# Kernel optimization log

Measured on AMD Instinct MI355X. Metric: run time of the kernel, lower is better.

The kernel has to match this reference:

```python
import jax, jax.numpy as jnp
import numpy as np

PLANES = ((0, 1), (0, 2), (0, 3), (1, 2), (1, 3), (2, 3))
LOOKBACK = 8
EPS = 1e-6


def phi(x):
    # LeakyReLU(negative_slope=0.01) + 1.0
    return jnp.where(x >= 0, x, 0.01 * x) + 1.0


def ga_embed(x, scalar_bias, vector_scale, vector_bias, bivector_weight):
    # x: [B, L, 4] -> M: [B, L, 11] = [scalar(1), vectors(4), bivectors(6)]
    scalar = jnp.broadcast_to(1.0 + scalar_bias, x.shape[:2] + (1,)).astype(x.dtype)
    vec = x * vector_scale + vector_bias
    biv = jnp.stack(
        [bivector_weight[k] * (x[..., i] - x[..., j]) for k, (i, j) in enumerate(PLANES)],
        axis=-1,
    )
    return jnp.concatenate([scalar, vec, biv], axis=-1)


def linear_attention(M, WQ, WK, WV):
    # Vectorized form of the per-timestep loop: for output t (t in [LOOKBACK, L)),
    # window is K/V[t-LOOKBACK : t]. q_t . S = sum_l (q_t . k_l) v_l, so we contract
    # scores first and never materialize the [B,T,H,H] S tensor.
    L = M.shape[1]
    T = L - LOOKBACK
    Q = phi(M @ WQ.T)   # [B, L, H]
    K = phi(M @ WK.T)
    V = M @ WV.T
    q = Q[:, LOOKBACK:]                                             # [B, T, H]
    K_win = jnp.stack([K[:, l:l + T] for l in range(LOOKBACK)], axis=2)  # [B, T, Lb, H]
    V_win = jnp.stack([V[:, l:l + T] for l in range(LOOKBACK)], axis=2)  # [B, T, Lb, H]
    scores = jnp.einsum('bth,btlh->btl', q, K_win)                  # [B, T, Lb]
    Z = K_win.sum(axis=2)                                           # [B, T, H]
    num = jnp.einsum('btl,btlg->btg', scores, V_win)                # [B, T, H]
    den = jnp.sum(q * Z, axis=-1, keepdims=True) + EPS
    contexts = num / den
    weights = scores / (jnp.sum(scores, axis=-1, keepdims=True) + EPS)
    return contexts, weights


def head_apply(ctx, head_W, head_b):
    # LinearHead: proj(H -> 1) then squeeze(-1)
    return (ctx @ head_W.T + head_b)[..., 0]


def qonly_delta(M, s0, s1, WQ, WK, WV, head_W, head_b):
    # _delta_y_query_only_fixed: last query t = L-1, window [t-Lb, t)
    Dm = M.shape[-1]
    q = phi(M[:, -1] @ WQ.T)                 # [B, H]
    win = M[:, -1 - LOOKBACK:-1]             # [B, Lb, Dm]
    k_win = phi(win @ WK.T)
    v_win = win @ WV.T
    S = jnp.einsum('blh,blg->bhg', k_win, v_win)   # [B, H, H] (small)
    Z = k_win.sum(axis=1)                           # [B, H]
    mask = jnp.zeros((Dm,), M.dtype).at[s0:s1].set(1.0)
    h_imp = (jnp.abs(WQ) * mask[None, :]).sum(axis=1)
    h_mask = h_imp / (h_imp.max() + 1e-12)
    q_masked = q * (1.0 - h_mask)

    def out(qv):
        num = jnp.einsum('bh,bhg->bg', qv, S)
        den = jnp.sum(qv * Z, axis=-1, keepdims=True) + EPS
        return head_apply(num / den, head_W, head_b)

    return jnp.abs(out(q) - out(q_masked)).mean()


def setup_inputs() -> dict:
    key = jax.random.key(0)
    ks = jax.random.split(key, 10)
    B, L, H, Dm = 16, 4096, 128, 11
    x = jax.random.normal(ks[0], (B, L, 4), dtype=jnp.float32)
    scalar_bias = 0.1 * jax.random.normal(ks[1], (1,), dtype=jnp.float32)
    vector_scale = 1.0 + 0.1 * jax.random.normal(ks[2], (4,), dtype=jnp.float32)
    vector_bias = 0.1 * jax.random.normal(ks[3], (4,), dtype=jnp.float32)
    bivector_weight = 1.0 + 0.1 * jax.random.normal(ks[4], (6,), dtype=jnp.float32)
    s = 1.0 / np.sqrt(Dm)
    WQ = s * jax.random.normal(ks[5], (H, Dm), dtype=jnp.float32)
    WK = s * jax.random.normal(ks[6], (H, Dm), dtype=jnp.float32)
    WV = s * jax.random.normal(ks[7], (H, Dm), dtype=jnp.float32)
    head_W = (1.0 / np.sqrt(H)) * jax.random.normal(ks[8], (1, H), dtype=jnp.float32)
    head_b = 0.1 * jax.random.normal(ks[9], (1,), dtype=jnp.float32)
    return {"x": x, "scalar_bias": scalar_bias, "vector_scale": vector_scale,
            "vector_bias": vector_bias, "bivector_weight": bivector_weight,
            "WQ": WQ, "WK": WK, "WV": WV, "head_W": head_W, "head_b": head_b}


def reference(x, scalar_bias, vector_scale, vector_bias, bivector_weight, WQ, WK, WV, head_W, head_b):
    M = ga_embed(x, scalar_bias, vector_scale, vector_bias, bivector_weight)
    contexts, attention_weights = linear_attention(M, WQ, WK, WV)
    predictions = head_apply(contexts, head_W, head_b)

    # interpretability (no_grad in the original)
    Ms = jax.lax.stop_gradient(M)
    scalar_mag = jnp.abs(Ms[..., 0]).mean()
    vector_mag = jnp.abs(Ms[..., 1:5]).mean()
    biv_mag = jnp.abs(Ms[..., 5:]).mean()

    def ablate_delta(Mz):
        ctx, _ = linear_attention(Mz, WQ, WK, WV)
        return jnp.abs(predictions - head_apply(ctx, head_W, head_b)).mean()

    delta_scalar = ablate_delta(Ms.at[..., 0].set(0.0))
    delta_vectors = ablate_delta(Ms.at[..., 1:5].set(0.0))
    delta_biv = ablate_delta(Ms.at[..., 5:].set(0.0))

    Dm = M.shape[-1]
    q_scalar = qonly_delta(Ms, 0, 1, WQ, WK, WV, head_W, head_b)
    q_vector = qonly_delta(Ms, 1, 5, WQ, WK, WV, head_W, head_b)
    q_biv = qonly_delta(Ms, 5, Dm, WQ, WK, WV, head_W, head_b)

    interpretability = jnp.stack([scalar_mag, vector_mag, biv_mag,
                                  delta_scalar, delta_vectors, delta_biv,
                                  q_scalar, q_vector, q_biv])
    return predictions, attention_weights, interpretability
```

## Files before the change

### kernel.cpp

```cpp
#include <hip/hip_runtime.h>

#define B_ 16
#define L_ 4096
#define H_ 128
#define DM 11
#define LB 8
#define T_ (L_-LB)
#define TT 64
#define NTB (L_/TT)
#define NBLK (NTB*B_)
#define EPSC 1e-6f
#define MAGS_BASE 4096
#define QONLY_BASE 8192


__device__ __forceinline__ float phi_f(float a) { return fmaxf(a, 0.01f * a) + 1.f; }

__device__ __forceinline__ float4 phi4(float a, float b, float c, float d) {
  return make_float4(phi_f(a), phi_f(b), phi_f(c), phi_f(d));
}

__device__ __forceinline__ void ga_parts(const float4 xv, const float* __restrict__ vs4,
                                         const float* __restrict__ vb4,
                                         const float* __restrict__ bw6, float* __restrict__ r) {
  r[0] = xv.x * vs4[0] + vb4[0];
  r[1] = xv.y * vs4[1] + vb4[1];
  r[2] = xv.z * vs4[2] + vb4[2];
  r[3] = xv.w * vs4[3] + vb4[3];
  r[4] = bw6[0] * (xv.x - xv.y);
  r[5] = bw6[1] * (xv.x - xv.z);
  r[6] = bw6[2] * (xv.x - xv.w);
  r[7] = bw6[3] * (xv.y - xv.z);
  r[8] = bw6[4] * (xv.y - xv.w);
  r[9] = bw6[5] * (xv.z - xv.w);
}

__device__ __forceinline__ void dot2(const float* __restrict__ r, const float* __restrict__ w,
                                     float& dv, float& db) {
  dv = r[0] * w[1] + r[1] * w[2] + r[2] * w[3] + r[3] * w[4];
  db = r[4] * w[5] + r[5] * w[6] + r[6] * w[7] + r[7] * w[8] + r[8] * w[9] + r[9] * w[10];
}

__global__ __launch_bounds__(256) void attn_kernel(
    const float* __restrict__ x, const float* __restrict__ sbp,
    const float* __restrict__ vs, const float* __restrict__ vb,
    const float* __restrict__ bw, const float* __restrict__ WQ,
    const float* __restrict__ WK, const float* __restrict__ WV,
    const float* __restrict__ hW, const float* __restrict__ hb,
    float* __restrict__ out, float* __restrict__ ws)
{
  __shared__ float4 sK4[4][8][72];
  __shared__ float4 sU4[72];
  __shared__ float  sWVe[16];

  const int tid  = threadIdx.x;
  const int lane = tid & 63;
  const int hq   = __builtin_amdgcn_readfirstlane(tid >> 6);
  const int tile = blockIdx.x;
  const int b    = blockIdx.y;
  const int base = tile * TT;

  const float sb0 = sbp[0];
  const float m0c = 1.f + sb0;
  float vs4[4] = {vs[0], vs[1], vs[2], vs[3]};
  float vb4[4] = {vb[0], vb[1], vb[2], vb[3]};
  float bw6[6] = {bw[0], bw[1], bw[2], bw[3], bw[4], bw[5]};
  const float hb0 = hb[0];

  const float4* xb = (const float4*)x + (size_t)b * L_;

  float ms[10], mq[10], m2[10];
  ga_parts(xb[base + lane], vs4, vb4, bw6, ms);
  {
    int qp = base + lane + LB;
    if (qp < L_) ga_parts(xb[qp], vs4, vb4, bw6, mq);
    else { for (int i = 0; i < 10; ++i) mq[i] = 0.f; }
  }
  const bool has2 = (lane < LB);
  if (has2) {
    int p2 = base + 64 + lane;
    if (p2 < L_) ga_parts(xb[p2], vs4, vb4, bw6, m2);
    else { for (int i = 0; i < 10; ++i) m2[i] = 0.f; }
  }
  float magv = fabsf(ms[0]) + fabsf(ms[1]) + fabsf(ms[2]) + fabsf(ms[3]);
  float magb = fabsf(ms[4]) + fabsf(ms[5]) + fabsf(ms[6]) + fabsf(ms[7]) + fabsf(ms[8]) + fabsf(ms[9]);

  if (hq == 1 && lane < DM) {
    float a = 0.f;
    for (int g = 0; g < H_; ++g) a += WV[g * DM + lane] * hW[g];
    sWVe[lane] = a;
  }
  __syncthreads();

  if (hq == 0) {
    float wv[11];
#pragma unroll
    for (int d = 0; d < DM; ++d) wv[d] = sWVe[d];
    float dv, db;
    dot2(ms, wv, dv, db);
    float c0 = m0c * wv[0];
    sU4[lane] = make_float4(c0 + dv + db, dv + db, c0 + db, c0 + dv);
    if (has2) {
      dot2(m2, wv, dv, db);
      sU4[64 + lane] = make_float4(c0 + dv + db, dv + db, c0 + db, c0 + dv);
    }
  }

  float4 s4[8];
#pragma unroll
  for (int l = 0; l < 8; ++l) s4[l] = make_float4(0.f, 0.f, 0.f, 0.f);

  const float* __restrict__ WKq = WK + (hq * 32) * DM;
  const float* __restrict__ WQq = WQ + (hq * 32) * DM;

#pragma unroll 1
  for (int c = 0; c < 4; ++c) {
#pragma unroll
    for (int hl = 0; hl < 8; ++hl) {
      const float* wk = WKq + (c * 8 + hl) * DM;
      float dv, db;
      dot2(ms, wk, dv, db);
      float c0 = m0c * wk[0];
      float t1 = dv + db;
      sK4[hq][hl][lane] = phi4(c0 + t1, t1, c0 + db, c0 + dv);
    }
    if (has2) {
#pragma unroll
      for (int hl = 0; hl < 8; ++hl) {
        const float* wk = WKq + (c * 8 + hl) * DM;
        float dv, db;
        dot2(m2, wk, dv, db);
        float c0 = m0c * wk[0];
        float t1 = dv + db;
        sK4[hq][hl][64 + lane] = phi4(c0 + t1, t1, c0 + db, c0 + dv);
      }
    }
    __syncthreads();
#pragma unroll
    for (int hl = 0; hl < 8; ++hl) {
      const float* wq = WQq + (c * 8 + hl) * DM;
      float dv, db;
      dot2(mq, wq, dv, db);
      float c0 = m0c * wq[0];
      float t1 = dv + db;
      float4 q4 = phi4(c0 + t1, t1, c0 + db, c0 + dv);
#pragma unroll
      for (int l = 0; l < 8; ++l) {
        float4 k4 = sK4[hq][hl][lane + l];
        s4[l].x += q4.x * k4.x;
        s4[l].y += q4.y * k4.y;
        s4[l].z += q4.z * k4.z;
        s4[l].w += q4.w * k4.w;
      }
    }
    __syncthreads();
  }

  float4* scr = &sK4[0][0][0];
  if (hq != 0) {
    int off = (hq - 1) * 512 + lane * 8;
#pragma unroll
    for (int l = 0; l < 8; ++l) scr[off + (l ^ (lane & 7))] = s4[l];
  }
  __syncthreads();

  if (hq == 0) {
#pragma unroll
    for (int j = 0; j < 3; ++j) {
      int off = j * 512 + lane * 8;
#pragma unroll
      for (int l = 0; l < 8; ++l) {
        float4 v = scr[off + (l ^ (lane & 7))];
        s4[l].x += v.x; s4[l].y += v.y; s4[l].z += v.z; s4[l].w += v.w;
      }
    }
    float den0 = EPSC, den1 = EPSC, den2 = EPSC, den3 = EPSC;
    float num0 = 0.f, num1 = 0.f, num2 = 0.f, num3 = 0.f;
#pragma unroll
    for (int l = 0; l < 8; ++l) {
      float4 u4 = sU4[lane + l];
      den0 += s4[l].x; num0 += s4[l].x * u4.x;
      den1 += s4[l].y; num1 += s4[l].y * u4.y;
      den2 += s4[l].z; num2 += s4[l].z * u4.z;
      den3 += s4[l].w; num3 += s4[l].w * u4.w;
    }
    float p0 = hb0 + num0 / den0;
    float p1 = hb0 + num1 / den1;
    float p2 = hb0 + num2 / den2;
    float p3 = hb0 + num3 / den3;

    const int t = base + lane;
    const bool tvalid = (t < T_);
    if (tvalid) {
      out[(size_t)b * T_ + t] = p0;
      float inv = 1.f / den0;
      float4* wp = (float4*)(out + (size_t)B_ * T_ + ((size_t)b * T_ + t) * 8);
      wp[0] = make_float4(s4[0].x * inv, s4[1].x * inv, s4[2].x * inv, s4[3].x * inv);
      wp[1] = make_float4(s4[4].x * inv, s4[5].x * inv, s4[6].x * inv, s4[7].x * inv);
    }
    float d1 = tvalid ? fabsf(p0 - p1) : 0.f;
    float d2 = tvalid ? fabsf(p0 - p2) : 0.f;
    float d3 = tvalid ? fabsf(p0 - p3) : 0.f;
#pragma unroll
    for (int off = 32; off >= 1; off >>= 1) {
      d1 += __shfl_xor(d1, off);
      d2 += __shfl_xor(d2, off);
      d3 += __shfl_xor(d3, off);
      magv += __shfl_xor(magv, off);
      magb += __shfl_xor(magb, off);
    }
    if (lane == 0) {
      int bid = b * NTB + tile;
      ws[bid]             = d1;
      ws[1024 + bid]      = d2;
      ws[2048 + bid]      = d3;
      ws[MAGS_BASE + 2 * bid]     = magv;
      ws[MAGS_BASE + 2 * bid + 1] = magb;
    }
  }

  if (hq == 1 && tile == NTB - 1) {
    const int h0 = lane, h1 = lane + 64;
    float wq0[11], wq1[11], wk0[11], wk1[11], wv[11];
#pragma unroll
    for (int d = 0; d < DM; ++d) {
      wq0[d] = WQ[h0 * DM + d]; wq1[d] = WQ[h1 * DM + d];
      wk0[d] = WK[h0 * DM + d]; wk1[d] = WK[h1 * DM + d];
      wv[d]  = sWVe[d];
    }
    float A0 = 0.f, Z0 = 0.f, A1 = 0.f, Z1 = 0.f;
#pragma unroll
    for (int l = 0; l < LB; ++l) {
      float4 xv = xb[L_ - 1 - LB + l];
      float r[10];
      ga_parts(xv, vs4, vb4, bw6, r);
      float uv, ub;
      dot2(r, wv, uv, ub);
      float u = m0c * wv[0] + uv + ub;
      float dv, db;
      dot2(r, wk0, dv, db);
      float k0 = phi_f(m0c * wk0[0] + dv + db);
      dot2(r, wk1, dv, db);
      float k1 = phi_f(m0c * wk1[0] + dv + db);
      A0 += k0 * u; Z0 += k0;
      A1 += k1 * u; Z1 += k1;
    }
    float q0, q1;
    {
      float4 xv = xb[L_ - 1];
      float r[10];
      ga_parts(xv, vs4, vb4, bw6, r);
      float dv, db;
      dot2(r, wq0, dv, db);
      q0 = phi_f(m0c * wq0[0] + dv + db);
      dot2(r, wq1, dv, db);
      q1 = phi_f(m0c * wq1[0] + dv + db);
    }
    float i00 = fabsf(wq0[0]);
    float i01 = fabsf(wq0[1]) + fabsf(wq0[2]) + fabsf(wq0[3]) + fabsf(wq0[4]);
    float i02 = fabsf(wq0[5]) + fabsf(wq0[6]) + fabsf(wq0[7]) + fabsf(wq0[8]) + fabsf(wq0[9]) + fabsf(wq0[10]);
    float i10 = fabsf(wq1[0]);
    float i11 = fabsf(wq1[1]) + fabsf(wq1[2]) + fabsf(wq1[3]) + fabsf(wq1[4]);
    float i12 = fabsf(wq1[5]) + fabsf(wq1[6]) + fabsf(wq1[7]) + fabsf(wq1[8]) + fabsf(wq1[9]) + fabsf(wq1[10]);
    float mm0 = fmaxf(i00, i10), mm1 = fmaxf(i01, i11), mm2 = fmaxf(i02, i12);
#pragma unroll
    for (int off = 32; off >= 1; off >>= 1) {
      mm0 = fmaxf(mm0, __shfl_xor(mm0, off));
      mm1 = fmaxf(mm1, __shfl_xor(mm1, off));
      mm2 = fmaxf(mm2, __shfl_xor(mm2, off));
    }
    mm0 += 1e-12f; mm1 += 1e-12f; mm2 += 1e-12f;
    float qa[4], qb_[4];
    qa[0] = q0;                      qb_[0] = q1;
    qa[1] = q0 * (1.f - i00 / mm0);  qb_[1] = q1 * (1.f - i10 / mm0);
    qa[2] = q0 * (1.f - i01 / mm1);  qb_[2] = q1 * (1.f - i11 / mm1);
    qa[3] = q0 * (1.f - i02 / mm2);  qb_[3] = q1 * (1.f - i12 / mm2);
    float num[4], den[4];
#pragma unroll
    for (int cc = 0; cc < 4; ++cc) {
      num[cc] = qa[cc] * A0 + qb_[cc] * A1;
      den[cc] = qa[cc] * Z0 + qb_[cc] * Z1;
    }
#pragma unroll
    for (int off = 32; off >= 1; off >>= 1) {
#pragma unroll
      for (int cc = 0; cc < 4; ++cc) {
        num[cc] += __shfl_xor(num[cc], off);
        den[cc] += __shfl_xor(den[cc], off);
      }
    }
    if (lane == 0) {
      float o0 = hb0 + num[0] / (den[0] + EPSC);
      float o1 = hb0 + num[1] / (den[1] + EPSC);
      float o2 = hb0 + num[2] / (den[2] + EPSC);
      float o3 = hb0 + num[3] / (den[3] + EPSC);
      ws[QONLY_BASE + b * 3 + 0] = fabsf(o0 - o1);
      ws[QONLY_BASE + b * 3 + 1] = fabsf(o0 - o2);
      ws[QONLY_BASE + b * 3 + 2] = fabsf(o0 - o3);
    }
  }
}

__global__ __launch_bounds__(64) void finalize_kernel(const float* __restrict__ ws,
                                                      const float* __restrict__ sbp,
                                                      float* __restrict__ out)
{
  int lane = threadIdx.x;
  float s0 = 0.f, s1 = 0.f, s2 = 0.f, mv = 0.f, bv = 0.f;
  for (int i = lane; i < NBLK; i += 64) {
    s0 += ws[i];
    s1 += ws[1024 + i];
    s2 += ws[2048 + i];
    mv += ws[MAGS_BASE + 2 * i];
    bv += ws[MAGS_BASE + 2 * i + 1];
  }
#pragma unroll
  for (int off = 32; off >= 1; off >>= 1) {
    s0 += __shfl_xor(s0, off);
    s1 += __shfl_xor(s1, off);
    s2 += __shfl_xor(s2, off);
    mv += __shfl_xor(mv, off);
    bv += __shfl_xor(bv, off);
  }
  if (lane == 0) {
    float q0 = 0.f, q1 = 0.f, q2 = 0.f;
    for (int b = 0; b < B_; ++b) {
      q0 += ws[QONLY_BASE + b * 3 + 0];
      q1 += ws[QONLY_BASE + b * 3 + 1];
      q2 += ws[QONLY_BASE + b * 3 + 2];
    }
    float* oi = out + (size_t)B_ * T_ + (size_t)B_ * T_ * 8;
    const float inv_bt = 1.f / ((float)B_ * (float)T_);
    oi[0] = fabsf(1.f + sbp[0]);
    oi[1] = mv / ((float)B_ * (float)L_ * 4.f);
    oi[2] = bv / ((float)B_ * (float)L_ * 6.f);
    oi[3] = s0 * inv_bt;
    oi[4] = s1 * inv_bt;
    oi[5] = s2 * inv_bt;
    oi[6] = q0 / (float)B_;
    oi[7] = q1 / (float)B_;
    oi[8] = q2 / (float)B_;
  }
}

extern "C" void kernel_launch(void* const* d_in, const int* in_sizes, int n_in,
                              void* d_out, int out_size, void* d_ws, size_t ws_size,
                              hipStream_t stream) {
  (void)in_sizes; (void)n_in; (void)out_size; (void)ws_size;
  const float* x  = (const float*)d_in[0];
  const float* sb = (const float*)d_in[1];
  const float* vs = (const float*)d_in[2];
  const float* vb = (const float*)d_in[3];
  const float* bw = (const float*)d_in[4];
  const float* WQ = (const float*)d_in[5];
  const float* WK = (const float*)d_in[6];
  const float* WV = (const float*)d_in[7];
  const float* hW = (const float*)d_in[8];
  const float* hb = (const float*)d_in[9];
  float* out = (float*)d_out;
  float* ws  = (float*)d_ws;

  attn_kernel<<<dim3(NTB, B_), 256, 0, stream>>>(x, sb, vs, vb, bw, WQ, WK, WV, hW, hb, out, ws);
  finalize_kernel<<<1, 64, 0, stream>>>(ws, sb, out);
}
```

Measured before the change: 81.36 us.

## Build halo keys from shifted query lanes and drop per-chunk block barriers

New measurement: 80.50 us. Within noise of the previous version (-1.1%).

```diff
diff --git a/kernel.cpp b/kernel.cpp
--- a/kernel.cpp
+++ b/kernel.cpp
@@ -69,19 +69,14 @@
 
   const float4* xb = (const float4*)x + (size_t)b * L_;
 
-  float ms[10], mq[10], m2[10];
+  float ms[10], mq[10];
   ga_parts(xb[base + lane], vs4, vb4, bw6, ms);
   {
     int qp = base + lane + LB;
     if (qp < L_) ga_parts(xb[qp], vs4, vb4, bw6, mq);
     else { for (int i = 0; i < 10; ++i) mq[i] = 0.f; }
   }
-  const bool has2 = (lane < LB);
-  if (has2) {
-    int p2 = base + 64 + lane;
-    if (p2 < L_) ga_parts(xb[p2], vs4, vb4, bw6, m2);
-    else { for (int i = 0; i < 10; ++i) m2[i] = 0.f; }
-  }
+  const bool hiLane = (lane >= 56);
   float magv = fabsf(ms[0]) + fabsf(ms[1]) + fabsf(ms[2]) + fabsf(ms[3]);
   float magb = fabsf(ms[4]) + fabsf(ms[5]) + fabsf(ms[6]) + fabsf(ms[7]) + fabsf(ms[8]) + fabsf(ms[9]);
 
@@ -100,9 +95,9 @@
     dot2(ms, wv, dv, db);
     float c0 = m0c * wv[0];
     sU4[lane] = make_float4(c0 + dv + db, dv + db, c0 + db, c0 + dv);
-    if (has2) {
-      dot2(m2, wv, dv, db);
-      sU4[64 + lane] = make_float4(c0 + dv + db, dv + db, c0 + db, c0 + dv);
+    if (hiLane) {
+      dot2(mq, wv, dv, db);
+      sU4[lane + 8] = make_float4(c0 + dv + db, dv + db, c0 + db, c0 + dv);
     }
   }
 
@@ -123,19 +118,13 @@
       float c0 = m0c * wk[0];
       float t1 = dv + db;
       sK4[hq][hl][lane] = phi4(c0 + t1, t1, c0 + db, c0 + dv);
-    }
-    if (has2) {
-#pragma unroll
-      for (int hl = 0; hl < 8; ++hl) {
-        const float* wk = WKq + (c * 8 + hl) * DM;
-        float dv, db;
-        dot2(m2, wk, dv, db);
-        float c0 = m0c * wk[0];
-        float t1 = dv + db;
-        sK4[hq][hl][64 + lane] = phi4(c0 + t1, t1, c0 + db, c0 + dv);
+      if (hiLane) {
+        float dv2, db2;
+        dot2(mq, wk, dv2, db2);
+        float t2 = dv2 + db2;
+        sK4[hq][hl][lane + 8] = phi4(c0 + t2, t2, c0 + db2, c0 + dv2);
       }
     }
-    __syncthreads();
 #pragma unroll
     for (int hl = 0; hl < 8; ++hl) {
       const float* wq = WQq + (c * 8 + hl) * DM;
@@ -153,9 +142,9 @@
         s4[l].w += q4.w * k4.w;
       }
     }
-    __syncthreads();
-  }
-
+  }
+
+  __syncthreads();
   float4* scr = &sK4[0][0][0];
   if (hq != 0) {
     int off = (hq - 1) * 512 + lane * 8;
```
